# Kernel tuning notes

Measured on AMD Instinct MI355X. Metric: run time of the kernel, lower is better.

The kernel has to match this reference:

```python
import jax, jax.numpy as jnp
import numpy as np

T, NNODES, DEG = 32, 10000, 32
IN_DIM, H1, HEADS, H2, GRU, PH = 128, 32, 4, 32, 32, 5


def setup_inputs() -> dict:
    key = jax.random.key(0)
    ks = jax.random.split(key, 24)
    d = {}
    d["h"] = jax.random.normal(ks[0], (T, NNODES, IN_DIM), jnp.float32)
    d["src"] = jax.random.randint(ks[1], (NNODES, DEG), 0, NNODES, dtype=jnp.int32)
    d["N"] = jnp.ones((1,), jnp.float32)
    d["I"] = jax.random.uniform(ks[2], (T,), jnp.float32)
    d["R"] = jax.random.uniform(ks[3], (T,), jnp.float32)
    d["S"] = jax.random.uniform(ks[4], (T,), jnp.float32)
    d["It"] = jax.random.uniform(ks[5], (T,), jnp.float32)
    d["Rt"] = jax.random.uniform(ks[6], (T,), jnp.float32)
    d["hx0"] = jax.random.normal(ks[7], (1, GRU), jnp.float32)
    # layer1: HEADS independent GATLayers (fc no-bias, attn_fc no-bias)
    d["W1"] = jax.random.normal(ks[8], (HEADS, IN_DIM, H1), jnp.float32) / np.sqrt(IN_DIM)
    d["a1"] = jax.random.normal(ks[9], (HEADS, 2 * H1), jnp.float32) / np.sqrt(2 * H1)
    # layer2: single head over concatenated features
    d["W2"] = jax.random.normal(ks[10], (1, HEADS * H1, H2), jnp.float32) / np.sqrt(HEADS * H1)
    d["a2"] = jax.random.normal(ks[11], (1, 2 * H2), jnp.float32) / np.sqrt(2 * H2)
    # GRUCell params (torch layout: W_ih [3*gru, in], W_hh [3*gru, gru])
    sg = 1.0 / np.sqrt(GRU)
    d["W_ih"] = jax.random.normal(ks[12], (3 * GRU, H2), jnp.float32) * sg
    d["W_hh"] = jax.random.normal(ks[13], (3 * GRU, GRU), jnp.float32) * sg
    d["b_ih"] = jax.random.normal(ks[14], (3 * GRU,), jnp.float32) * sg
    d["b_hh"] = jax.random.normal(ks[15], (3 * GRU,), jnp.float32) * sg
    sr = 1.0 / np.sqrt(GRU + 2)
    d["Wr1"] = jax.random.normal(ks[16], (2 * PH, GRU + 2), jnp.float32) * sr
    d["br1"] = jax.random.normal(ks[17], (2 * PH,), jnp.float32) * sr
    d["Wr2"] = jax.random.normal(ks[18], (2, GRU + 2), jnp.float32) * sr
    d["br2"] = jax.random.normal(ks[19], (2,), jnp.float32) * sr
    return d


def _gat(x, W, a, src):
    # x: [n, din]; W: [H, din, dout]; a: [H, 2*dout]; src: [n, D] in-neighbor ids
    dout = W.shape[-1]
    z = jnp.einsum('nd,hde->hne', x, W)                    # [H, n, dout]
    zs = z[:, src]                                          # [H, n, D, dout] mailbox of src feats
    e = (jnp.einsum('hnde,he->hnd', zs, a[:, :dout])        # a . z_src part
         + jnp.einsum('hne,he->hn', z, a[:, dout:])[:, :, None])  # a . z_dst part
    alpha = jax.nn.softmax(jax.nn.leaky_relu(e, 0.01), axis=-1)   # softmax over mailbox dim
    return jnp.einsum('hnd,hnde->hne', alpha, zs)           # [H, n, dout]


def reference(h, src, N, I, R, S, It, Rt, hx0, W1, a1, W2, a2,
              W_ih, W_hh, b_ih, b_hh, Wr1, br1, Wr2, br2):
    n = h.shape[1]
    Ns = N.squeeze()

    def step(hx, xs):
        iz, I_t, R_t, S_t, It_t, Rt_t = xs
        h1 = jax.nn.relu(_gat(iz, W1, a1, src))             # [H, n, H1]
        h1 = jnp.transpose(h1, (1, 0, 2)).reshape(n, -1)    # cat heads -> [n, H*H1]
        h2 = _gat(h1, W2, a2, src)[0]                       # [n, H2]
        cur = jnp.max(jax.nn.relu(h2), axis=0)[None, :]     # [1, H2]
        # GRUCell
        gi = cur @ W_ih.T + b_ih
        gh = hx @ W_hh.T + b_hh
        gir, giz, gin = jnp.split(gi, 3, axis=1)
        ghr, ghz, ghn = jnp.split(gh, 3, axis=1)
        r = jax.nn.sigmoid(gir + ghr)
        zg = jax.nn.sigmoid(giz + ghz)
        ng = jnp.tanh(gin + r * ghn)
        hx_new = (1.0 - zg) * ng + zg * hx                  # [1, GRU]
        new_hx = jnp.concatenate([hx_new, It_t.reshape(1, 1), Rt_t.reshape(1, 1)], axis=1)
        pred = (new_hx @ Wr1.T + br1).squeeze()             # [2*PH]
        ab = (new_hx @ Wr2.T + br2).squeeze()               # [2]
        a_s = jax.nn.sigmoid(ab[0])
        b_s = jax.nn.sigmoid(ab[1])
        new_I_t = pred[0::2]
        new_R_t = pred[1::2]
        # SIR physics rollout with detached recurrence
        last_I, last_R, last_S = I_t, R_t, S_t
        phyI, phyR = [], []
        dI = jnp.zeros(())
        dR = jnp.zeros(())
        for i in range(PH):
            if i > 0:
                last_I = last_I + jax.lax.stop_gradient(dI)
                last_R = last_R + jax.lax.stop_gradient(dR)
                last_S = Ns - last_I - last_R
            dI = a_s * last_I * (last_S / Ns) - b_s * last_I
            dR = b_s * last_I
            phyI.append(dI)
            phyR.append(dR)
        return hx_new, (new_I_t, new_R_t, jnp.stack(phyI), jnp.stack(phyR))

    _, (nI, nR, pI, pR) = jax.lax.scan(step, hx0, (h, I, R, S, It, Rt))
    return nI, nR, pI.reshape(-1), pR.reshape(-1)
```

## Files before the change

### kernel.cpp

```cpp
#include <hip/hip_runtime.h>

typedef __attribute__((ext_vector_type(8))) short short8;
typedef __attribute__((ext_vector_type(4))) float floatx4;
typedef __attribute__((ext_vector_type(2))) float float2v;
typedef __attribute__((ext_vector_type(4))) unsigned int uint4v;
typedef __attribute__((ext_vector_type(4))) int int4v;
typedef __attribute__((ext_vector_type(2))) unsigned int uint2v;

__device__ __forceinline__ float bf2f(unsigned short u) {
    return __uint_as_float(((unsigned int)u) << 16);
}
__device__ __forceinline__ unsigned short f2bf(float f) {
    unsigned int x = __float_as_uint(f);
    unsigned int r = (x + 0x7FFFu + ((x >> 16) & 1u)) >> 16;
    return (unsigned short)r;
}
__device__ __forceinline__ float ldf(const void* p, long i, bool f32) {
    return f32 ? ((const float*)p)[i] : bf2f(((const unsigned short*)p)[i]);
}
__device__ __forceinline__ bool detect_f32(const unsigned short* Nv) {
    return Nv[0] == 0;
}

template<int CTRL>
__device__ __forceinline__ float dppf(float x) {
    return __int_as_float(__builtin_amdgcn_update_dpp(
        0, __float_as_int(x), CTRL, 0xF, 0xF, true));
}
__device__ __forceinline__ float swz16(float x) {
    return __int_as_float(__builtin_amdgcn_ds_swizzle(__float_as_int(x), 0x401F));
}
__device__ __forceinline__ float red32max(float x) {
    x = fmaxf(x, dppf<0x128>(x));
    x = fmaxf(x, dppf<0x124>(x));
    x = fmaxf(x, dppf<0x122>(x));
    x = fmaxf(x, dppf<0x121>(x));
    return fmaxf(x, swz16(x));
}
__device__ __forceinline__ float red32sum(float x) {
    x += dppf<0x128>(x);
    x += dppf<0x124>(x);
    x += dppf<0x122>(x);
    x += dppf<0x121>(x);
    return x + swz16(x);
}
__device__ __forceinline__ float addx8_dpp(float x) {
    return x + dppf<0x128>(x);
}

template<int SEL>
__device__ __forceinline__ void pkfma2(float2v& acc, unsigned int z, float2v ap) {
    float2v x;
    x[0] = __uint_as_float(z << 16);
    x[1] = __uint_as_float(z & 0xffff0000u);
    if (SEL == 0)
        asm("v_pk_fma_f32 %0, %1, %2, %0 op_sel:[0,0,0] op_sel_hi:[1,0,1]"
            : "+v"(acc) : "v"(x), "v"(ap));
    else
        asm("v_pk_fma_f32 %0, %1, %2, %0 op_sel:[0,1,0] op_sel_hi:[1,1,1]"
            : "+v"(acc) : "v"(x), "v"(ap));
}

#define P_WIH 0
#define P_WHH 3072
#define P_BIH 6144
#define P_BHH 6240
#define P_WR1 6336
#define P_BR1 6676
#define P_WR2 6686
#define P_BR2 6754
#define P_I   6756
#define P_R   6788
#define P_S   6820
#define P_IT  6852
#define P_RT  6884
#define P_N   6916
#define P_HX0 6917
#define P_TOT 6949

__global__ __launch_bounds__(256) void norm_params(
    const void* W1, const void* a1, const void* W2, const void* a2,
    const void* W_ih, const void* W_hh, const void* b_ih, const void* b_hh,
    const void* Wr1, const void* br1, const void* Wr2, const void* br2,
    const void* Iv, const void* Rv, const void* Sv, const void* Itv, const void* Rtv,
    const void* Nv, const void* hx0,
    float* __restrict__ P, unsigned short* __restrict__ WbT1,
    unsigned short* __restrict__ WbT2)
{
    bool f32 = detect_f32((const unsigned short*)Nv);
    int tid = threadIdx.x;
    struct Item { const void* p; int n; int off; };
    const Item items[15] = {
        {W_ih, 3072, P_WIH}, {W_hh, 3072, P_WHH}, {b_ih, 96, P_BIH}, {b_hh, 96, P_BHH},
        {Wr1, 340, P_WR1}, {br1, 10, P_BR1}, {Wr2, 68, P_WR2}, {br2, 2, P_BR2},
        {Iv, 32, P_I}, {Rv, 32, P_R}, {Sv, 32, P_S}, {Itv, 32, P_IT}, {Rtv, 32, P_RT},
        {Nv, 1, P_N}, {hx0, 32, P_HX0}
    };
    for (int it = 0; it < 15; it++)
        for (int i = tid; i < items[it].n; i += 256)
            P[items[it].off + i] = ldf(items[it].p, i, f32);

    for (int idx = tid; idx < 144 * 128; idx += 256) {
        int col = idx >> 7, k = idx & 127;
        float v = 0.f;
        if (col < 128) {
            int h = col >> 5, e = col & 31;
            v = ldf(W1, (h * 128 + k) * 32 + e, f32);
        } else if (col < 136) {
            int q = col - 128;
            int h = (q < 4) ? q : q - 4;
            int off = (q < 4) ? 0 : 32;
            float s = 0.f;
            for (int e = 0; e < 32; e++)
                s += ldf(W1, (h * 128 + k) * 32 + e, f32) * ldf(a1, h * 64 + off + e, f32);
            v = s;
        }
        WbT1[col * 128 + k] = f2bf(v);
    }
    for (int idx = tid; idx < 48 * 128; idx += 256) {
        int col = idx >> 7, k = idx & 127;
        float v = 0.f;
        if (col < 32) {
            v = ldf(W2, k * 32 + col, f32);
        } else if (col < 34) {
            int off = (col == 32) ? 0 : 32;
            float s = 0.f;
            for (int e = 0; e < 32; e++)
                s += ldf(W2, k * 32 + e, f32) * ldf(a2, off + e, f32);
            v = s;
        }
        WbT2[col * 128 + k] = f2bf(v);
    }
}

template<int NT, int HC, bool DYN>
__global__ __launch_bounds__(256) void gat_linear(
    const void* __restrict__ Xv, const unsigned short* __restrict__ WbT,
    unsigned short* __restrict__ Z, float* __restrict__ EL, float* __restrict__ ER,
    const unsigned short* __restrict__ Nv, long row0)
{
    constexpr int NCOL = NT * 16;
    constexpr int LDW  = 136;
    __shared__ unsigned short Ws[NCOL * LDW];
    int tid = threadIdx.x;
    for (int idx = tid; idx < NCOL * 16; idx += 256) {
        int col = idx >> 4, ch = idx & 15;
        *(uint4v*)(&Ws[col * LDW + ch * 8]) = *(const uint4v*)(&WbT[col * 128 + ch * 8]);
    }
    __syncthreads();

    bool f32 = DYN ? detect_f32(Nv) : false;
    int wave = tid >> 6, lane = tid & 63;
    int l15 = lane & 15, quad = lane >> 4;
    long lrow = (long)blockIdx.x * 64 + wave * 16;

    floatx4 acc[NT];
    floatx4 zz = {0.f, 0.f, 0.f, 0.f};
    #pragma unroll
    for (int i = 0; i < NT; i++) acc[i] = zz;

    long xoff = (row0 + lrow + l15) * 128 + quad * 8;
    #pragma unroll
    for (int kt = 0; kt < 4; kt++) {
        short8 afrag;
        if (DYN && f32) {
            const float* xr = (const float*)Xv + xoff + kt * 32;
            float4 u0 = ((const float4*)xr)[0];
            float4 u1 = ((const float4*)xr)[1];
            union { short8 v; unsigned short u[8]; } af;
            af.u[0] = f2bf(u0.x); af.u[1] = f2bf(u0.y);
            af.u[2] = f2bf(u0.z); af.u[3] = f2bf(u0.w);
            af.u[4] = f2bf(u1.x); af.u[5] = f2bf(u1.y);
            af.u[6] = f2bf(u1.z); af.u[7] = f2bf(u1.w);
            afrag = af.v;
        } else {
            afrag = *(const short8*)((const unsigned short*)Xv + xoff + kt * 32);
        }
        #pragma unroll
        for (int nt = 0; nt < NT; nt++) {
            short8 bfrag = *(const short8*)(&Ws[(nt * 16 + l15) * LDW + kt * 32 + quad * 8]);
            acc[nt] = __builtin_amdgcn_mfma_f32_16x16x32_bf16(afrag, bfrag, acc[nt], 0, 0, 0);
        }
    }

    #pragma unroll
    for (int nt = 0; nt < NT; nt++) {
        int col = nt * 16 + l15;
        #pragma unroll
        for (int r = 0; r < 4; r++) {
            long grow = lrow + quad * 4 + r;
            float v = acc[nt][r];
            if (col < HC * 32) {
                Z[grow * (HC * 32) + col] = f2bf(v);
            } else if (col < HC * 32 + HC) {
                EL[grow * HC + (col - HC * 32)] = v;
            } else if (col < HC * 32 + 2 * HC) {
                ER[grow * HC + (col - HC * 32 - HC)] = v;
            }
        }
    }
}

__device__ __forceinline__ void iss8(uint4v* buf, const int4v sa, const int4v sb,
                                     const char* Zb, unsigned fb) {
    #pragma unroll
    for (int k = 0; k < 4; k++)
        buf[k] = *(const uint4v*)(Zb + (unsigned)(sa[k] * 256) + fb);
    #pragma unroll
    for (int k = 0; k < 4; k++)
        buf[4 + k] = *(const uint4v*)(Zb + (unsigned)(sb[k] * 256) + fb);
}
__device__ __forceinline__ void cons8(const uint4v* buf, const floatx4 ax, const floatx4 ay,
                                      float2v& c0, float2v& c1, float2v& c2, float2v& c3) {
    float2v a01 = {ax[0], ax[1]};
    float2v a23 = {ax[2], ax[3]};
    float2v a45 = {ay[0], ay[1]};
    float2v a67 = {ay[2], ay[3]};
    #define STEP(K, AP, SEL)              \
        pkfma2<SEL>(c0, buf[K].x, AP);    \
        pkfma2<SEL>(c1, buf[K].y, AP);    \
        pkfma2<SEL>(c2, buf[K].z, AP);    \
        pkfma2<SEL>(c3, buf[K].w, AP);
    STEP(0, a01, 0) STEP(1, a01, 1)
    STEP(2, a23, 0) STEP(3, a23, 1)
    STEP(4, a45, 0) STEP(5, a45, 1)
    STEP(6, a67, 0) STEP(7, a67, 1)
    #undef STEP
}

__global__ __launch_bounds__(256, 5) void gat1_aggr(
    const int* __restrict__ src,
    const unsigned short* __restrict__ Z,
    const float* __restrict__ EL,
    const float* __restrict__ ER,
    unsigned short* __restrict__ H1,
    int NX)
{
    __shared__ float als[4][4][4][36];
    __shared__ int   sid[4][4][32];
    int tid = threadIdx.x;
    int w = tid >> 6, lane = tid & 63;
    int d31 = lane & 31, hf = lane >> 5;

    int bid = blockIdx.x;
    int xcd = bid % NX;
    int j   = bid / NX;
    int tq  = j / 625;
    int r   = j - tq * 625;
    int t   = tq * NX + xcd;
    int tb  = t * 10000;
    int n0  = r * 16 + w * 4;
    const char* Zb = (const char*)Z + (size_t)tb * 256;

    int sidx[4];
    #pragma unroll
    for (int jj = 0; jj < 4; jj++)
        sidx[jj] = src[(n0 + jj) * 32 + d31];

    int mA = hf ? sidx[1] : sidx[0];
    int mB = hf ? sidx[3] : sidx[2];
    floatx4 elA = *(const floatx4*)(EL + (size_t)(tb + mA) * 4);
    floatx4 elB = *(const floatx4*)(EL + (size_t)(tb + mB) * 4);
    floatx4 erA = *(const floatx4*)(ER + (size_t)(tb + n0 + hf) * 4);
    floatx4 erB = *(const floatx4*)(ER + (size_t)(tb + n0 + 2 + hf) * 4);

    float xA[4], xB[4];
    #pragma unroll
    for (int h = 0; h < 4; h++) {
        float a = elA[h] + erA[h];
        float b = elB[h] + erB[h];
        a = a >= 0.f ? a : 0.01f * a;
        b = b >= 0.f ? b : 0.01f * b;
        xA[h] = __expf(a - red32max(a));
        xB[h] = __expf(b - red32max(b));
    }
    #pragma unroll
    for (int h = 0; h < 4; h++) {
        als[w][hf][h][d31]     = xA[h] * __builtin_amdgcn_rcpf(red32sum(xA[h]));
        als[w][2 + hf][h][d31] = xB[h] * __builtin_amdgcn_rcpf(red32sum(xB[h]));
    }
    if (hf == 0) {
        #pragma unroll
        for (int jj = 0; jj < 4; jj++)
            sid[w][jj][d31] = sidx[jj];
    }
    __builtin_amdgcn_wave_barrier();

    int u = lane >> 4;
    int f = lane & 15;
    int h = f >> 2;
    unsigned fb = (unsigned)f * 16u;

    {
        int jj = u;
        const int* sp = &sid[w][jj][0];
        int4v sv0 = *(const int4v*)(sp + 0);
        int4v sv1 = *(const int4v*)(sp + 4);
        int4v sv2 = *(const int4v*)(sp + 8);
        int4v sv3 = *(const int4v*)(sp + 12);
        int4v sv4 = *(const int4v*)(sp + 16);
        int4v sv5 = *(const int4v*)(sp + 20);
        int4v sv6 = *(const int4v*)(sp + 24);
        int4v sv7 = *(const int4v*)(sp + 28);

        uint4v zA[8], zB[8];
        iss8(zA, sv0, sv1, Zb, fb);
        iss8(zB, sv2, sv3, Zb, fb);

        const float* ap_ = &als[w][jj][h][0];
        floatx4 av0 = *(const floatx4*)(ap_ + 0);
        floatx4 av1 = *(const floatx4*)(ap_ + 4);
        floatx4 av2 = *(const floatx4*)(ap_ + 8);
        floatx4 av3 = *(const floatx4*)(ap_ + 12);
        floatx4 av4 = *(const floatx4*)(ap_ + 16);
        floatx4 av5 = *(const floatx4*)(ap_ + 20);
        floatx4 av6 = *(const floatx4*)(ap_ + 24);
        floatx4 av7 = *(const floatx4*)(ap_ + 28);

        float2v c0 = {0.f, 0.f}, c1 = {0.f, 0.f}, c2 = {0.f, 0.f}, c3 = {0.f, 0.f};
        cons8(zA, av0, av1, c0, c1, c2, c3);
        iss8(zA, sv4, sv5, Zb, fb);
        cons8(zB, av2, av3, c0, c1, c2, c3);
        iss8(zB, sv6, sv7, Zb, fb);
        cons8(zA, av4, av5, c0, c1, c2, c3);
        cons8(zB, av6, av7, c0, c1, c2, c3);

        int n = n0 + jj;
        float p0 = fmaxf(c0[0], 0.f), p1 = fmaxf(c0[1], 0.f);
        float p2 = fmaxf(c1[0], 0.f), p3 = fmaxf(c1[1], 0.f);
        float p4 = fmaxf(c2[0], 0.f), p5 = fmaxf(c2[1], 0.f);
        float p6 = fmaxf(c3[0], 0.f), p7 = fmaxf(c3[1], 0.f);
        unsigned r0, r1, r2, r3;
        asm("v_cvt_pk_bf16_f32 %0, %1, %2" : "=v"(r0) : "v"(p0), "v"(p1));
        asm("v_cvt_pk_bf16_f32 %0, %1, %2" : "=v"(r1) : "v"(p2), "v"(p3));
        asm("v_cvt_pk_bf16_f32 %0, %1, %2" : "=v"(r2) : "v"(p4), "v"(p5));
        asm("v_cvt_pk_bf16_f32 %0, %1, %2" : "=v"(r3) : "v"(p6), "v"(p7));
        uint4v o = {r0, r1, r2, r3};
        __builtin_nontemporal_store(o,
            (uint4v*)((char*)H1 + (size_t)(tb + n) * 256 + fb));
    }
}

__global__ __launch_bounds__(256, 4) void gat2_aggr(
    const int* __restrict__ src,
    const unsigned short* __restrict__ Z2,
    const float* __restrict__ EL2,
    const float* __restrict__ ER2,
    int* __restrict__ cur, int t0, int NX)
{
    __shared__ float als2[4][8][32];
    __shared__ int bm[32];
    int tid = threadIdx.x, w = tid >> 6, lane = tid & 63;
    int d31 = lane & 31, g = lane >> 5;
    int g3 = lane >> 3, f7 = lane & 7;

    int bid = blockIdx.x;
    int xcd = bid % NX;
    int j   = bid / NX;
    int tq  = j / 157;
    int r   = j - tq * 157;
    int t   = tq * NX + xcd;
    int tb  = t * 10000;
    int n0  = r * 64 + w * 16;
    const char* Zb = (const char*)Z2 + (size_t)tb * 64;

    if (tid < 32) bm[tid] = 0;
    __syncthreads();

    float m4[4] = {0.f, 0.f, 0.f, 0.f};
    #pragma unroll
    for (int b = 0; b < 2; b++) {
        int nb = n0 + b * 8;
        float xv[4];
        #pragma unroll
        for (int k = 0; k < 4; k++) {
            int n = nb + 2 * k + g;
            n = n > 9999 ? 9999 : n;
            int m = src[n * 32 + d31];
            float e = EL2[tb + m] + ER2[tb + n];
            e = e >= 0.f ? e : 0.01f * e;
            xv[k] = __expf(e - red32max(e));
        }
        #pragma unroll
        for (int k = 0; k < 4; k++)
            als2[w][2 * k + g][d31] = xv[k] * __builtin_amdgcn_rcpf(red32sum(xv[k]));
        __builtin_amdgcn_wave_barrier();

        #pragma unroll
        for (int jj = 0; jj < 8; jj++) {
            int n = nb + jj;
            if (n >= 10000) continue;
            floatx4 av4 = *(const floatx4*)&als2[w][jj][g3 * 4];
            int4v mv = *(const int4v*)(src + n * 32 + g3 * 4);
            uint2v ldv[4];
            #pragma unroll
            for (int k = 0; k < 4; k++)
                ldv[k] = *(const uint2v*)(Zb + (unsigned int)(mv[k] * 64 + f7 * 8));
            float2v a01 = {av4[0], av4[1]};
            float2v a23 = {av4[2], av4[3]};
            float2v c01 = {0.f, 0.f}, c23 = {0.f, 0.f};
            pkfma2<0>(c01, ldv[0].x, a01); pkfma2<0>(c23, ldv[0].y, a01);
            pkfma2<1>(c01, ldv[1].x, a01); pkfma2<1>(c23, ldv[1].y, a01);
            pkfma2<0>(c01, ldv[2].x, a23); pkfma2<0>(c23, ldv[2].y, a23);
            pkfma2<1>(c01, ldv[3].x, a23); pkfma2<1>(c23, ldv[3].y, a23);
            float c0 = c01[0], c1 = c01[1], c2 = c23[0], c3 = c23[1];
            c0 = addx8_dpp(c0); c1 = addx8_dpp(c1);
            c2 = addx8_dpp(c2); c3 = addx8_dpp(c3);
            c0 += swz16(c0); c1 += swz16(c1);
            c2 += swz16(c2); c3 += swz16(c3);
            c0 += __shfl_xor(c0, 32);
            c1 += __shfl_xor(c1, 32);
            c2 += __shfl_xor(c2, 32);
            c3 += __shfl_xor(c3, 32);
            m4[0] = fmaxf(m4[0], c0);
            m4[1] = fmaxf(m4[1], c1);
            m4[2] = fmaxf(m4[2], c2);
            m4[3] = fmaxf(m4[3], c3);
        }
        __builtin_amdgcn_wave_barrier();
    }
    if (lane < 8) {
        #pragma unroll
        for (int i = 0; i < 4; i++)
            atomicMax(&bm[f7 * 4 + i], __float_as_int(m4[i]));
    }
    __syncthreads();
    if (tid < 32) atomicMax(&cur[(t0 + t) * 32 + tid], bm[tid]);
}

__global__ __launch_bounds__(128) void gru_head(
    const float* __restrict__ P, const float* __restrict__ cur,
    void* __restrict__ outv, const unsigned short* __restrict__ Nv)
{
    bool f32 = detect_f32(Nv);
    __shared__ float Whh[96 * 32], giAll[32 * 96];
    __shared__ float hx[32], gh[96], nh[34];
    int tid = threadIdx.x;
    for (int i = tid; i < 96 * 32; i += 128)
        Whh[i] = P[P_WHH + i];
    for (int o = tid; o < 32 * 96; o += 128) {
        int t = o / 96, gg = o - t * 96;
        float s = P[P_BIH + gg];
        for (int k = 0; k < 32; k++)
            s += cur[t * 32 + k] * P[P_WIH + gg * 32 + k];
        giAll[o] = s;
    }
    if (tid < 32) hx[tid] = P[P_HX0 + tid];
    __syncthreads();

    for (int t = 0; t < 32; t++) {
        if (tid < 96) {
            float sh = 0.f;
            for (int k = 0; k < 32; k++)
                sh += hx[k] * Whh[tid * 32 + k];
            gh[tid] = sh + P[P_BHH + tid];
        }
        __syncthreads();
        if (tid < 32) {
            const float* gi = &giAll[t * 96];
            float r  = 1.f / (1.f + __expf(-(gi[tid] + gh[tid])));
            float zg = 1.f / (1.f + __expf(-(gi[32 + tid] + gh[32 + tid])));
            float ng = tanhf(gi[64 + tid] + r * gh[64 + tid]);
            float hv = (1.f - zg) * ng + zg * hx[tid];
            hx[tid] = hv;
            nh[tid] = hv;
            if (tid == 0) { nh[32] = P[P_IT + t]; nh[33] = P[P_RT + t]; }
        }
        __syncthreads();
        if (tid < 10) {
            float s = P[P_BR1 + tid];
            for (int k = 0; k < 34; k++) s += nh[k] * P[P_WR1 + tid * 34 + k];
            int i = tid >> 1;
            int oi = ((tid & 1) == 0) ? (t * 5 + i) : (160 + t * 5 + i);
            if (f32) ((float*)outv)[oi] = s;
            else     ((unsigned short*)outv)[oi] = f2bf(s);
        }
        if (tid == 64) {
            float ab0 = P[P_BR2 + 0], ab1 = P[P_BR2 + 1];
            for (int k = 0; k < 34; k++) {
                ab0 += nh[k] * P[P_WR2 + k];
                ab1 += nh[k] * P[P_WR2 + 34 + k];
            }
            float a_s = 1.f / (1.f + __expf(-ab0));
            float b_s = 1.f / (1.f + __expf(-ab1));
            float Ns = P[P_N];
            float lI = P[P_I + t], lR = P[P_R + t], lS = P[P_S + t];
            float dI = 0.f, dR = 0.f;
            for (int i = 0; i < 5; i++) {
                if (i > 0) { lI += dI; lR += dR; lS = Ns - lI - lR; }
                dI = a_s * lI * (lS / Ns) - b_s * lI;
                dR = b_s * lI;
                if (f32) {
                    ((float*)outv)[320 + t * 5 + i] = dI;
                    ((float*)outv)[480 + t * 5 + i] = dR;
                } else {
                    ((unsigned short*)outv)[320 + t * 5 + i] = f2bf(dI);
                    ((unsigned short*)outv)[480 + t * 5 + i] = f2bf(dR);
                }
            }
        }
        __syncthreads();
    }
}

extern "C" void kernel_launch(void* const* d_in, const int* in_sizes, int n_in,
                              void* d_out, int out_size, void* d_ws, size_t ws_size,
                              hipStream_t stream) {
    const void* h    = d_in[0];
    const int*  src  = (const int*)d_in[1];
    const void* Nv   = d_in[2];
    const void* Iv   = d_in[3];
    const void* Rv   = d_in[4];
    const void* Sv   = d_in[5];
    const void* Itv  = d_in[6];
    const void* Rtv  = d_in[7];
    const void* hx0  = d_in[8];
    const void* W1   = d_in[9];
    const void* a1   = d_in[10];
    const void* W2   = d_in[11];
    const void* a2   = d_in[12];
    const void* W_ih = d_in[13];
    const void* W_hh = d_in[14];
    const void* b_ih = d_in[15];
    const void* b_hh = d_in[16];
    const void* Wr1  = d_in[17];
    const void* br1  = d_in[18];
    const void* Wr2  = d_in[19];
    const void* br2  = d_in[20];
    const unsigned short* Nu = (const unsigned short*)Nv;

    int TC = 4;
    for (int c = 32; c >= 4; c >>= 1) {
        size_t need = (size_t)c * 10000 * (128 * 2 + 128 * 2 + 16 + 16) + (1 << 20);
        if (need <= ws_size) { TC = c; break; }
    }
    long CR = (long)TC * 10000;

    char* ws = (char*)d_ws;
    size_t off = 0;
    auto alloc = [&](size_t b) {
        void* p = ws + off;
        off += (b + 255) & ~(size_t)255;
        return p;
    };
    float*          Pb   = (float*)alloc(P_TOT * 4);
    unsigned short* WbT1 = (unsigned short*)alloc(144 * 128 * 2);
    unsigned short* WbT2 = (unsigned short*)alloc(48 * 128 * 2);
    float*          cur  = (float*)alloc(32 * 32 * 4);
    unsigned short* z1   = (unsigned short*)alloc((size_t)CR * 128 * 2);
    unsigned short* h1   = (unsigned short*)alloc((size_t)CR * 128 * 2);
    float*          el1  = (float*)alloc((size_t)CR * 4 * 4);
    float*          er1  = (float*)alloc((size_t)CR * 4 * 4);
    unsigned short* z2   = z1;
    float*          el2  = el1;
    float*          er2  = er1;

    (void)hipMemsetAsync(cur, 0, 32 * 32 * 4, stream);
    norm_params<<<1, 256, 0, stream>>>(W1, a1, W2, a2, W_ih, W_hh, b_ih, b_hh,
                                       Wr1, br1, Wr2, br2, Iv, Rv, Sv, Itv, Rtv,
                                       Nv, hx0, Pb, WbT1, WbT2);
    int nchunks = 32 / TC;
    int g1 = (int)(CR / 64);
    int NX = TC < 8 ? TC : 8;
    int TQ = TC / NX;
    for (int c = 0; c < nchunks; c++) {
        long row0 = (long)c * CR;
        gat_linear<9, 4, true><<<g1, 256, 0, stream>>>(h, WbT1, z1, el1, er1, Nu, row0);
        gat1_aggr<<<NX * 625 * TQ, 256, 0, stream>>>(src, z1, el1, er1, h1, NX);
        gat_linear<3, 1, false><<<g1, 256, 0, stream>>>(h1, WbT2, z2, el2, er2, Nu, 0);
        gat2_aggr<<<NX * 157 * TQ, 256, 0, stream>>>(src, z2, el2, er2, (int*)cur, c * TC, NX);
    }
    gru_head<<<1, 128, 0, stream>>>(Pb, cur, d_out, Nu);
}
```

Before: 632.8 us.

## Restructure gat2 aggregation to one node per lane group and parallelize param prep

gat2_aggr now caches each node's neighbour ids alongside the softmax weights in shared memory. Each 8-lane group then handles a whole node across all 32 neighbours, with software-pipelined gathers. This replaces the per-node cross-lane sum reductions with a single max reduction at the end and removes the repeated global src reloads. norm_params is also launched over 48 blocks instead of one to cut its serial prologue time. The new layout uses more LDS and more registers per wave.

```diff
diff --git a/kernel.cpp b/kernel.cpp
--- a/kernel.cpp
+++ b/kernel.cpp
@@ -43,9 +43,6 @@
     x += dppf<0x122>(x);
     x += dppf<0x121>(x);
     return x + swz16(x);
-}
-__device__ __forceinline__ float addx8_dpp(float x) {
-    return x + dppf<0x128>(x);
 }
 
 template<int SEL>
@@ -88,7 +85,8 @@
     unsigned short* __restrict__ WbT2)
 {
     bool f32 = detect_f32((const unsigned short*)Nv);
-    int tid = threadIdx.x;
+    int gtid = blockIdx.x * 256 + threadIdx.x;
+    int gstr = gridDim.x * 256;
     struct Item { const void* p; int n; int off; };
     const Item items[15] = {
         {W_ih, 3072, P_WIH}, {W_hh, 3072, P_WHH}, {b_ih, 96, P_BIH}, {b_hh, 96, P_BHH},
@@ -97,10 +95,10 @@
         {Nv, 1, P_N}, {hx0, 32, P_HX0}
     };
     for (int it = 0; it < 15; it++)
-        for (int i = tid; i < items[it].n; i += 256)
+        for (int i = gtid; i < items[it].n; i += gstr)
             P[items[it].off + i] = ldf(items[it].p, i, f32);
 
-    for (int idx = tid; idx < 144 * 128; idx += 256) {
+    for (int idx = gtid; idx < 144 * 128; idx += gstr) {
         int col = idx >> 7, k = idx & 127;
         float v = 0.f;
         if (col < 128) {
@@ -117,7 +115,7 @@
         }
         WbT1[col * 128 + k] = f2bf(v);
     }
-    for (int idx = tid; idx < 48 * 128; idx += 256) {
+    for (int idx = gtid; idx < 48 * 128; idx += gstr) {
         int col = idx >> 7, k = idx & 127;
         float v = 0.f;
         if (col < 32) {
@@ -341,6 +339,31 @@
     }
 }
 
+__device__ __forceinline__ void iss8b(uint2v* buf, const int4v sa, const int4v sb,
+                                      const char* Zb, unsigned fb) {
+    #pragma unroll
+    for (int k = 0; k < 4; k++)
+        buf[k] = *(const uint2v*)(Zb + (unsigned)(sa[k] * 64) + fb);
+    #pragma unroll
+    for (int k = 0; k < 4; k++)
+        buf[4 + k] = *(const uint2v*)(Zb + (unsigned)(sb[k] * 64) + fb);
+}
+__device__ __forceinline__ void cons8b(const uint2v* buf, const floatx4 ax, const floatx4 ay,
+                                       float2v& c01, float2v& c23) {
+    float2v a01 = {ax[0], ax[1]};
+    float2v a23 = {ax[2], ax[3]};
+    float2v a45 = {ay[0], ay[1]};
+    float2v a67 = {ay[2], ay[3]};
+    pkfma2<0>(c01, buf[0].x, a01); pkfma2<0>(c23, buf[0].y, a01);
+    pkfma2<1>(c01, buf[1].x, a01); pkfma2<1>(c23, buf[1].y, a01);
+    pkfma2<0>(c01, buf[2].x, a23); pkfma2<0>(c23, buf[2].y, a23);
+    pkfma2<1>(c01, buf[3].x, a23); pkfma2<1>(c23, buf[3].y, a23);
+    pkfma2<0>(c01, buf[4].x, a45); pkfma2<0>(c23, buf[4].y, a45);
+    pkfma2<1>(c01, buf[5].x, a45); pkfma2<1>(c23, buf[5].y, a45);
+    pkfma2<0>(c01, buf[6].x, a67); pkfma2<0>(c23, buf[6].y, a67);
+    pkfma2<1>(c01, buf[7].x, a67); pkfma2<1>(c23, buf[7].y, a67);
+}
+
 __global__ __launch_bounds__(256, 4) void gat2_aggr(
     const int* __restrict__ src,
     const unsigned short* __restrict__ Z2,
@@ -348,11 +371,12 @@
     const float* __restrict__ ER2,
     int* __restrict__ cur, int t0, int NX)
 {
-    __shared__ float als2[4][8][32];
+    __shared__ float als2[4][16][36];
+    __shared__ int   sid2[4][16][36];
     __shared__ int bm[32];
     int tid = threadIdx.x, w = tid >> 6, lane = tid & 63;
     int d31 = lane & 31, g = lane >> 5;
-    int g3 = lane >> 3, f7 = lane & 7;
+    int u3 = lane >> 3, f7 = lane & 7;
 
     int bid = blockIdx.x;
     int xcd = bid % NX;
@@ -367,62 +391,83 @@
     if (tid < 32) bm[tid] = 0;
     __syncthreads();
 
-    float m4[4] = {0.f, 0.f, 0.f, 0.f};
     #pragma unroll
     for (int b = 0; b < 2; b++) {
         int nb = n0 + b * 8;
-        float xv[4];
+        float xv[4]; int sv[4];
         #pragma unroll
         for (int k = 0; k < 4; k++) {
             int n = nb + 2 * k + g;
             n = n > 9999 ? 9999 : n;
-            int m = src[n * 32 + d31];
-            float e = EL2[tb + m] + ER2[tb + n];
+            sv[k] = src[n * 32 + d31];
+            float e = EL2[tb + sv[k]] + ER2[tb + n];
             e = e >= 0.f ? e : 0.01f * e;
             xv[k] = __expf(e - red32max(e));
         }
         #pragma unroll
-        for (int k = 0; k < 4; k++)
-            als2[w][2 * k + g][d31] = xv[k] * __builtin_amdgcn_rcpf(red32sum(xv[k]));
-        __builtin_amdgcn_wave_barrier();
-
-        #pragma unroll
-        for (int jj = 0; jj < 8; jj++) {
-            int n = nb + jj;
-            if (n >= 10000) continue;
-            floatx4 av4 = *(const floatx4*)&als2[w][jj][g3 * 4];
-            int4v mv = *(const int4v*)(src + n * 32 + g3 * 4);
-            uint2v ldv[4];
-            #pragma unroll
-            for (int k = 0; k < 4; k++)
-                ldv[k] = *(const uint2v*)(Zb + (unsigned int)(mv[k] * 64 + f7 * 8));
-            float2v a01 = {av4[0], av4[1]};
-            float2v a23 = {av4[2], av4[3]};
-            float2v c01 = {0.f, 0.f}, c23 = {0.f, 0.f};
-            pkfma2<0>(c01, ldv[0].x, a01); pkfma2<0>(c23, ldv[0].y, a01);
-            pkfma2<1>(c01, ldv[1].x, a01); pkfma2<1>(c23, ldv[1].y, a01);
-            pkfma2<0>(c01, ldv[2].x, a23); pkfma2<0>(c23, ldv[2].y, a23);
-            pkfma2<1>(c01, ldv[3].x, a23); pkfma2<1>(c23, ldv[3].y, a23);
-            float c0 = c01[0], c1 = c01[1], c2 = c23[0], c3 = c23[1];
-            c0 = addx8_dpp(c0); c1 = addx8_dpp(c1);
-            c2 = addx8_dpp(c2); c3 = addx8_dpp(c3);
-            c0 += swz16(c0); c1 += swz16(c1);
-            c2 += swz16(c2); c3 += swz16(c3);
-            c0 += __shfl_xor(c0, 32);
-            c1 += __shfl_xor(c1, 32);
-            c2 += __shfl_xor(c2, 32);
-            c3 += __shfl_xor(c3, 32);
-            m4[0] = fmaxf(m4[0], c0);
-            m4[1] = fmaxf(m4[1], c1);
-            m4[2] = fmaxf(m4[2], c2);
-            m4[3] = fmaxf(m4[3], c3);
-        }
-        __builtin_amdgcn_wave_barrier();
-    }
+        for (int k = 0; k < 4; k++) {
+            int slot = b * 8 + 2 * k + g;
+            als2[w][slot][d31] = xv[k] * __builtin_amdgcn_rcpf(red32sum(xv[k]));
+            sid2[w][slot][d31] = sv[k];
+        }
+    }
+    __builtin_amdgcn_wave_barrier();
+
+    unsigned fb = (unsigned)f7 * 8u;
+    float2v m01 = {0.f, 0.f}, m23 = {0.f, 0.f};
+    #pragma unroll
+    for (int b = 0; b < 2; b++) {
+        int jj = b * 8 + u3;
+        const int* sp = &sid2[w][jj][0];
+        int4v sv0 = *(const int4v*)(sp + 0);
+        int4v sv1 = *(const int4v*)(sp + 4);
+        int4v sv2 = *(const int4v*)(sp + 8);
+        int4v sv3 = *(const int4v*)(sp + 12);
+        int4v sv4 = *(const int4v*)(sp + 16);
+        int4v sv5 = *(const int4v*)(sp + 20);
+        int4v sv6 = *(const int4v*)(sp + 24);
+        int4v sv7 = *(const int4v*)(sp + 28);
+
+        uint2v zA[8], zB[8];
+        iss8b(zA, sv0, sv1, Zb, fb);
+        iss8b(zB, sv2, sv3, Zb, fb);
+
+        const float* ap_ = &als2[w][jj][0];
+        floatx4 av0 = *(const floatx4*)(ap_ + 0);
+        floatx4 av1 = *(const floatx4*)(ap_ + 4);
+        floatx4 av2 = *(const floatx4*)(ap_ + 8);
+        floatx4 av3 = *(const floatx4*)(ap_ + 12);
+        floatx4 av4 = *(const floatx4*)(ap_ + 16);
+        floatx4 av5 = *(const floatx4*)(ap_ + 20);
+        floatx4 av6 = *(const floatx4*)(ap_ + 24);
+        floatx4 av7 = *(const floatx4*)(ap_ + 28);
+
+        float2v c01 = {0.f, 0.f}, c23 = {0.f, 0.f};
+        cons8b(zA, av0, av1, c01, c23);
+        iss8b(zA, sv4, sv5, Zb, fb);
+        cons8b(zB, av2, av3, c01, c23);
+        iss8b(zB, sv6, sv7, Zb, fb);
+        cons8b(zA, av4, av5, c01, c23);
+        cons8b(zB, av6, av7, c01, c23);
+
+        m01[0] = fmaxf(m01[0], c01[0]);
+        m01[1] = fmaxf(m01[1], c01[1]);
+        m23[0] = fmaxf(m23[0], c23[0]);
+        m23[1] = fmaxf(m23[1], c23[1]);
+    }
+
+    float c0 = m01[0], c1 = m01[1], c2 = m23[0], c3 = m23[1];
+    c0 = fmaxf(c0, dppf<0x128>(c0)); c1 = fmaxf(c1, dppf<0x128>(c1));
+    c2 = fmaxf(c2, dppf<0x128>(c2)); c3 = fmaxf(c3, dppf<0x128>(c3));
+    c0 = fmaxf(c0, swz16(c0)); c1 = fmaxf(c1, swz16(c1));
+    c2 = fmaxf(c2, swz16(c2)); c3 = fmaxf(c3, swz16(c3));
+    c0 = fmaxf(c0, __shfl_xor(c0, 32)); c1 = fmaxf(c1, __shfl_xor(c1, 32));
+    c2 = fmaxf(c2, __shfl_xor(c2, 32)); c3 = fmaxf(c3, __shfl_xor(c3, 32));
     if (lane < 8) {
-        #pragma unroll
-        for (int i = 0; i < 4; i++)
-            atomicMax(&bm[f7 * 4 + i], __float_as_int(m4[i]));
+        atomicMax(&bm[f7 * 4 + 0], __float_as_int(c0));
+        atomicMax(&bm[f7 * 4 + 1], __float_as_int(c1));
+        atomicMax(&bm[f7 * 4 + 2], __float_as_int(c2));
+        atomicMax(&bm[f7 * 4 + 3], __float_as_int(c3));
     }
     __syncthreads();
     if (tid < 32) atomicMax(&cur[(t0 + t) * 32 + tid], bm[tid]);
@@ -556,9 +601,9 @@
     float*          er2  = er1;
 
     (void)hipMemsetAsync(cur, 0, 32 * 32 * 4, stream);
-    norm_params<<<1, 256, 0, stream>>>(W1, a1, W2, a2, W_ih, W_hh, b_ih, b_hh,
-                                       Wr1, br1, Wr2, br2, Iv, Rv, Sv, Itv, Rtv,
-                                       Nv, hx0, Pb, WbT1, WbT2);
+    norm_params<<<48, 256, 0, stream>>>(W1, a1, W2, a2, W_ih, W_hh, b_ih, b_hh,
+                                        Wr1, br1, Wr2, br2, Iv, Rv, Sv, Itv, Rtv,
+                                        Nv, hx0, Pb, WbT1, WbT2);
     int nchunks = 32 / TC;
     int g1 = (int)(CR / 64);
     int NX = TC < 8 ? TC : 8;
```

New measurement: 587.7 us. -7.1%, faster.
